# Kernel optimization log

Hardware: AMD Instinct MI355X
Metric: run time of the kernel (lower is better)

## Reference

```python
import jax, jax.numpy as jnp
import numpy as np
from jax import lax


def _pairwise_dist(a, b):
    # a: (T, D), b: (T, D) -> (T, T) Euclidean distances via GEMM trick
    a2 = jnp.sum(a * a, axis=-1)
    b2 = jnp.sum(b * b, axis=-1)
    sq = a2[:, None] + b2[None, :] - 2.0 * (a @ b.T)
    return jnp.sqrt(jnp.maximum(sq, 1e-12))


def _frechet(seq1, seq2):
    cost = _pairwise_dist(seq1, seq2)  # (T, T)
    ca0 = lax.cummax(cost[0])          # first row boundary: running max

    def row_step(prev, cost_row):
        # prev: ca[i-1, :]; cost_row: cost[i, :]
        c0 = jnp.maximum(prev[0], cost_row[0])  # first-column boundary

        def col_step(left, x):
            c, up, diag = x
            val = jnp.maximum(c, jnp.minimum(jnp.minimum(up, left), diag))
            return val, val

        _, rest = lax.scan(col_step, c0, (cost_row[1:], prev[1:], prev[:-1]))
        cur = jnp.concatenate([c0[None], rest])
        return cur, None

    final_row, _ = lax.scan(row_step, ca0, cost[1:])
    return final_row[-1]


def setup_inputs() -> dict:
    key = jax.random.key(0)
    k1, k2 = jax.random.split(key)
    B, T, D = 32, 1024, 64
    pred = jax.random.normal(k1, (B, T, D), dtype=jnp.float32)
    targ = jax.random.normal(k2, (B, T, D), dtype=jnp.float32)
    return {"pred": pred, "targ": targ}


def reference(pred, targ):
    dists = jax.vmap(_frechet)(pred, targ)  # (B,)
    return jnp.mean(dists)
```

## Files before the change

### kernel.cpp

```cpp
#include <hip/hip_runtime.h>
#include <hip/hip_fp16.h>
#include <hip/hip_bf16.h>
#include <math.h>

#define T_LEN 1024
#define D_DIM 64
#define BATCH 32

#define SLACK_FRONT 64
#define SLACK_BACK  72
#define ROW_STRIDE  (T_LEN + SLACK_FRONT)
#define PD 8

typedef __attribute__((ext_vector_type(2))) _Float16 h2v;

__global__ __launch_bounds__(256) void fill_slack_kernel(__half* __restrict__ ws) {
    int g = blockIdx.x * 256 + threadIdx.x;
    int b = g >> 13;
    int off = g & 8191;
    uint4* dst = (uint4*)(ws + (size_t)b * ((size_t)ROW_STRIDE * T_LEN)) + off;
    *dst = make_uint4(0x7C007C00u, 0x7C007C00u, 0x7C007C00u, 0x7C007C00u);
}

__global__ __launch_bounds__(256) void cost_kernel(const float* __restrict__ pred,
                                                   const float* __restrict__ targ,
                                                   __half* __restrict__ cost_base,
                                                   unsigned long long batch_stride_h) {
    const int b = blockIdx.z;
    const float* P = pred + (size_t)b * T_LEN * D_DIM;
    const float* T = targ + (size_t)b * T_LEN * D_DIM;
    __half* C = cost_base + (size_t)b * batch_stride_h;
    const int row0 = blockIdx.y * 128;
    const int col0 = blockIdx.x * 128;

    __shared__ __align__(16) float ps[32][132];
    __shared__ __align__(16) float ts[32][132];
    __shared__ float p2[128], t2[128];

    const int tid = threadIdx.x;

    {
        int r = tid & 127;
        const float* src = (tid < 128) ? (P + (size_t)(row0 + r) * D_DIM)
                                       : (T + (size_t)(col0 + r) * D_DIM);
        float s = 0.0f;
#pragma unroll
        for (int q = 0; q < 16; q++) {
            float4 v = ((const float4*)src)[q];
            s += v.x * v.x + v.y * v.y + v.z * v.z + v.w * v.w;
        }
        if (tid < 128) p2[r] = s; else t2[r] = s;
    }

    const int lane = tid & 63, wv = tid >> 6;
    const int TX = (lane & 7) + 8 * (wv & 1);
    const int TY = (lane >> 3) + 8 * (wv >> 1);

    float acc[8][8];
#pragma unroll
    for (int i = 0; i < 8; i++)
#pragma unroll
        for (int j = 0; j < 8; j++) acc[i][j] = 0.0f;

#pragma unroll
    for (int chunk = 0; chunk < 2; ++chunk) {
        __syncthreads();
#pragma unroll
        for (int it = 0; it < 4; ++it) {
            int idx = tid + 256 * it;
            int row = idx >> 3;
            int kc = idx & 7;
            float4 v = *(const float4*)(P + (size_t)(row0 + row) * D_DIM + 32 * chunk + 4 * kc);
            ps[4 * kc + 0][row] = v.x; ps[4 * kc + 1][row] = v.y;
            ps[4 * kc + 2][row] = v.z; ps[4 * kc + 3][row] = v.w;
            float4 w = *(const float4*)(T + (size_t)(col0 + row) * D_DIM + 32 * chunk + 4 * kc);
            ts[4 * kc + 0][row] = w.x; ts[4 * kc + 1][row] = w.y;
            ts[4 * kc + 2][row] = w.z; ts[4 * kc + 3][row] = w.w;
        }
        __syncthreads();

#pragma unroll
        for (int kk = 0; kk < 32; ++kk) {
            float4 a0 = *(const float4*)&ps[kk][8 * TY];
            float4 a1 = *(const float4*)&ps[kk][8 * TY + 4];
            float4 b0 = *(const float4*)&ts[kk][8 * TX];
            float4 b1 = *(const float4*)&ts[kk][8 * TX + 4];
            float av[8] = {a0.x, a0.y, a0.z, a0.w, a1.x, a1.y, a1.z, a1.w};
            float bv[8] = {b0.x, b0.y, b0.z, b0.w, b1.x, b1.y, b1.z, b1.w};
#pragma unroll
            for (int i = 0; i < 8; i++)
#pragma unroll
                for (int j = 0; j < 8; j++) acc[i][j] += av[i] * bv[j];
        }
    }
    __syncthreads();

#pragma unroll
    for (int i = 0; i < 8; i++) {
        float pa = p2[8 * TY + i];
        h2v o2[4];
#pragma unroll
        for (int j = 0; j < 4; j++) {
            float d0 = pa + t2[8 * TX + 2 * j]     - 2.0f * acc[i][2 * j];
            float d1 = pa + t2[8 * TX + 2 * j + 1] - 2.0f * acc[i][2 * j + 1];
            h2v h;
            h[0] = (_Float16)sqrtf(fmaxf(d0, 1e-12f));
            h[1] = (_Float16)sqrtf(fmaxf(d1, 1e-12f));
            o2[j] = h;
        }
        float4 st;
        st.x = __builtin_bit_cast(float, o2[0]);
        st.y = __builtin_bit_cast(float, o2[1]);
        st.z = __builtin_bit_cast(float, o2[2]);
        st.w = __builtin_bit_cast(float, o2[3]);
        __half* dst = C + (size_t)(row0 + 8 * TY + i) * T_LEN + col0 + 8 * TX;
        *(float4*)dst = st;
    }
}


#define CELL(c_, pv_) { \
    float c = (c_); \
    float e = fminf(pv_, diag); \
    float hm = fmaxf(e, c); \
    float vv = __builtin_amdgcn_fmed3f(c, hm, left); \
    diag = pv_; pv_ = vv; left = vv; }

#define DP_STEP(PA, PB) { \
    float inc = __shfl_up(right_out, 1, 64); \
    float left = (t == 0) ? lane0_left : inc; \
    float diag = (t == 0) ? INF : diag_feed; \
    diag_feed = inc; \
    h2v u0 = __builtin_bit_cast(h2v, PA.x), u1 = __builtin_bit_cast(h2v, PA.y); \
    h2v u2 = __builtin_bit_cast(h2v, PA.z), u3 = __builtin_bit_cast(h2v, PA.w); \
    h2v u4 = __builtin_bit_cast(h2v, PB.x), u5 = __builtin_bit_cast(h2v, PB.y); \
    h2v u6 = __builtin_bit_cast(h2v, PB.z), u7 = __builtin_bit_cast(h2v, PB.w); \
    CELL((float)u0[0], v0)  CELL((float)u0[1], v1) \
    CELL((float)u1[0], v2)  CELL((float)u1[1], v3) \
    CELL((float)u2[0], v4)  CELL((float)u2[1], v5) \
    CELL((float)u3[0], v6)  CELL((float)u3[1], v7) \
    CELL((float)u4[0], v8)  CELL((float)u4[1], v9) \
    CELL((float)u5[0], v10) CELL((float)u5[1], v11) \
    CELL((float)u6[0], v12) CELL((float)u6[1], v13) \
    CELL((float)u7[0], v14) CELL((float)u7[1], v15) \
    right_out = left; lane0_left = INF; }

#define RELOAD(n) { \
    const float4* p4 = (const float4*)q##n; \
    a##n = p4[0]; b##n = p4[1]; \
    q##n += (size_t)PD * T_LEN; }

#define INIT_SLOT(n) { \
    const float4* p4 = (const float4*)(Cl + (ptrdiff_t)(n - t) * T_LEN); \
    a##n = p4[0]; b##n = p4[1]; \
    q##n = Cl + (ptrdiff_t)(n + PD - t) * T_LEN; }

__global__ __launch_bounds__(64, 1) void dp_kernel_nb(const __half* __restrict__ cost,
                                                      float* __restrict__ out) {
    const int b = blockIdx.x;
    const int t = threadIdx.x;
    const float INF = __builtin_inff();
    const __half* Cl = cost + ((size_t)SLACK_FRONT + (size_t)b * ROW_STRIDE) * T_LEN + 16 * t;

    float v0 = INF, v1 = INF, v2 = INF, v3 = INF, v4 = INF, v5 = INF, v6 = INF, v7 = INF;
    float v8 = INF, v9 = INF, v10 = INF, v11 = INF, v12 = INF, v13 = INF, v14 = INF, v15 = INF;
    float right_out = INF;
    float diag_feed = INF;
    float lane0_left = -INF;

    float4 a0, b0, a1, b1, a2, b2, a3, b3, a4, b4, a5, b5, a6, b6, a7, b7;
    const __half *q0, *q1, *q2, *q3, *q4, *q5, *q6, *q7;
    INIT_SLOT(0) INIT_SLOT(1) INIT_SLOT(2) INIT_SLOT(3)
    INIT_SLOT(4) INIT_SLOT(5) INIT_SLOT(6) INIT_SLOT(7)

    for (int chunk = 0; chunk < 135; ++chunk) {
        DP_STEP(a0, b0) RELOAD(0)
        DP_STEP(a1, b1) RELOAD(1)
        DP_STEP(a2, b2) RELOAD(2)
        DP_STEP(a3, b3) RELOAD(3)
        DP_STEP(a4, b4) RELOAD(4)
        DP_STEP(a5, b5) RELOAD(5)
        DP_STEP(a6, b6) RELOAD(6)
        DP_STEP(a7, b7) RELOAD(7)
    }
    DP_STEP(a0, b0)
    DP_STEP(a1, b1)
    DP_STEP(a2, b2)
    DP_STEP(a3, b3)
    DP_STEP(a4, b4)
    DP_STEP(a5, b5)
    DP_STEP(a6, b6)

    if (t == 63) atomicAdd(out, v15 * (1.0f / (float)BATCH));
}

__global__ __launch_bounds__(64) void dp_fused_kernel(const float* __restrict__ pred,
                                                      const float* __restrict__ targ,
                                                      float* __restrict__ out) {
    const int b = blockIdx.x;
    const int t = threadIdx.x;
    const float INF = __builtin_inff();
    const float* P = pred + (size_t)b * T_LEN * D_DIM;
    const float* T = targ + (size_t)b * T_LEN * D_DIM + (size_t)(16 * t) * D_DIM;

    float prev[16];
#pragma unroll
    for (int j = 0; j < 16; j++) prev[j] = INF;
    float right_out = INF;
    float diag_feed = INF;

    for (int s = 0; s < T_LEN + 63; s++) {
        int r = s - t;
        float inc = __shfl_up(right_out, 1, 64);
        float left = inc, diag = diag_feed;
        diag_feed = inc;
        if (t == 0) { left = (r == 0) ? -INF : INF; diag = INF; }
        if (r >= 0 && r < T_LEN) {
            float4 pr[16];
            const float4* pp = (const float4*)(P + (size_t)r * D_DIM);
#pragma unroll
            for (int q = 0; q < 16; q++) pr[q] = pp[q];
#pragma unroll
            for (int j = 0; j < 16; j++) {
                const float4* tp = (const float4*)(T + (size_t)j * D_DIM);
                float acc = 0.0f;
#pragma unroll
                for (int q = 0; q < 16; q++) {
                    float4 tv = tp[q];
                    float dx = pr[q].x - tv.x; acc += dx * dx;
                    float dy = pr[q].y - tv.y; acc += dy * dy;
                    float dz = pr[q].z - tv.z; acc += dz * dz;
                    float dw = pr[q].w - tv.w; acc += dw * dw;
                }
                float c = sqrtf(fmaxf(acc, 1e-12f));
                float e = fminf(prev[j], diag);
                float hm = fmaxf(e, c);
                float vv = __builtin_amdgcn_fmed3f(c, hm, left);
                diag = prev[j];
                prev[j] = vv;
                left = vv;
            }
            right_out = left;
        }
    }
    if (t == 63) atomicAdd(out, prev[15] * (1.0f / (float)BATCH));
}

extern "C" void kernel_launch(void* const* d_in, const int* in_sizes, int n_in,
                              void* d_out, int out_size, void* d_ws, size_t ws_size,
                              hipStream_t stream) {
    const float* pred = (const float*)d_in[0];
    const float* targ = (const float*)d_in[1];
    float* out = (float*)d_out;

    hipMemsetAsync(out, 0, sizeof(float) * out_size, stream);

    const size_t need_strided =
        ((size_t)BATCH * ROW_STRIDE + SLACK_BACK) * (size_t)T_LEN * sizeof(__half);

    if (ws_size >= need_strided) {
        __half* ws = (__half*)d_ws;
        fill_slack_kernel<<<1024, 256, 0, stream>>>(ws);
        __half* cost_base = ws + (size_t)SLACK_FRONT * T_LEN;
        dim3 grid(8, 8, BATCH);
        cost_kernel<<<grid, 256, 0, stream>>>(pred, targ, cost_base,
                                              (unsigned long long)ROW_STRIDE * T_LEN);
        dp_kernel_nb<<<BATCH, 64, 0, stream>>>(ws, out);
    } else {
        dp_fused_kernel<<<BATCH, 64, 0, stream>>>(pred, targ, out);
    }
}
```

Measured before the change: 368.5 us.

## Skew cost matrix storage, run DP recurrence in fp16, pin reload scheduling

The cost kernel now writes each 16-column strip shifted down by its lane index, so every DP wavefront step reads one contiguous skewed row. Only the upper-left staircase is filled with +inf, which replaces the full slack-fill pass. The DP recurrence now keeps its state in _Float16 with half min/max/med3 operations and shuffles 16-bit values, and sched_barriers fence each reload. Doing the min/max in fp16 could change rounding and ties compared with the fp32 path, and the fused fallback swaps fmed3 for a max/min pair.

```diff
diff --git a/kernel.cpp b/kernel.cpp
--- a/kernel.cpp
+++ b/kernel.cpp
@@ -1,35 +1,58 @@
 #include <hip/hip_runtime.h>
 #include <hip/hip_fp16.h>
-#include <hip/hip_bf16.h>
 #include <math.h>
 
 #define T_LEN 1024
 #define D_DIM 64
 #define BATCH 32
 
-#define SLACK_FRONT 64
-#define SLACK_BACK  72
-#define ROW_STRIDE  (T_LEN + SLACK_FRONT)
+#define SKEW_ROWS 1104
+#define SKEW_STRIDE ((size_t)SKEW_ROWS * T_LEN)
 #define PD 8
 
 typedef __attribute__((ext_vector_type(2))) _Float16 h2v;
 
-__global__ __launch_bounds__(256) void fill_slack_kernel(__half* __restrict__ ws) {
-    int g = blockIdx.x * 256 + threadIdx.x;
-    int b = g >> 13;
-    int off = g & 8191;
-    uint4* dst = (uint4*)(ws + (size_t)b * ((size_t)ROW_STRIDE * T_LEN)) + off;
-    *dst = make_uint4(0x7C007C00u, 0x7C007C00u, 0x7C007C00u, 0x7C007C00u);
+static __device__ __forceinline__ _Float16 hmin_(_Float16 a, _Float16 b) {
+#if __has_builtin(__builtin_fminf16)
+    return __builtin_fminf16(a, b);
+#else
+    return (b < a) ? b : a;
+#endif
+}
+static __device__ __forceinline__ _Float16 hmax_(_Float16 a, _Float16 b) {
+#if __has_builtin(__builtin_fmaxf16)
+    return __builtin_fmaxf16(a, b);
+#else
+    return (a < b) ? b : a;
+#endif
+}
+static __device__ __forceinline__ _Float16 med3h_(_Float16 a, _Float16 b, _Float16 c) {
+#if __has_builtin(__builtin_amdgcn_fmed3h)
+    return __builtin_amdgcn_fmed3h(a, b, c);
+#else
+    return hmax_(a, hmin_(b, c));
+#endif
+}
+
+__global__ __launch_bounds__(128) void fill_stairs_kernel(__half* __restrict__ ws) {
+    int s = blockIdx.x;
+    int b = blockIdx.y;
+    int tid = threadIdx.x;
+    int col0 = 16 * (s + 1);
+    int n_u4 = (T_LEN - col0) >> 3;
+    if (tid < n_u4) {
+        __half* row = ws + (size_t)b * SKEW_STRIDE + (size_t)s * T_LEN + col0;
+        ((uint4*)row)[tid] = make_uint4(0x7C007C00u, 0x7C007C00u, 0x7C007C00u, 0x7C007C00u);
+    }
 }
 
 __global__ __launch_bounds__(256) void cost_kernel(const float* __restrict__ pred,
                                                    const float* __restrict__ targ,
-                                                   __half* __restrict__ cost_base,
-                                                   unsigned long long batch_stride_h) {
+                                                   __half* __restrict__ skew_base) {
     const int b = blockIdx.z;
     const float* P = pred + (size_t)b * T_LEN * D_DIM;
     const float* T = targ + (size_t)b * T_LEN * D_DIM;
-    __half* C = cost_base + (size_t)b * batch_stride_h;
+    __half* C = skew_base + (size_t)b * SKEW_STRIDE;
     const int row0 = blockIdx.y * 128;
     const int col0 = blockIdx.x * 128;
 
@@ -95,6 +118,7 @@
     }
     __syncthreads();
 
+    const int skew = (col0 >> 4) + (TX >> 1);
 #pragma unroll
     for (int i = 0; i < 8; i++) {
         float pa = p2[8 * TY + i];
@@ -113,66 +137,67 @@
         st.y = __builtin_bit_cast(float, o2[1]);
         st.z = __builtin_bit_cast(float, o2[2]);
         st.w = __builtin_bit_cast(float, o2[3]);
-        __half* dst = C + (size_t)(row0 + 8 * TY + i) * T_LEN + col0 + 8 * TX;
+        __half* dst = C + (size_t)(row0 + 8 * TY + i + skew) * T_LEN + col0 + 8 * TX;
         *(float4*)dst = st;
     }
 }
 
 
 #define CELL(c_, pv_) { \
-    float c = (c_); \
-    float e = fminf(pv_, diag); \
-    float hm = fmaxf(e, c); \
-    float vv = __builtin_amdgcn_fmed3f(c, hm, left); \
+    _Float16 c = (c_); \
+    _Float16 e = hmin_(pv_, diag); \
+    _Float16 hm = hmax_(e, c); \
+    _Float16 vv = med3h_(c, hm, left); \
     diag = pv_; pv_ = vv; left = vv; }
 
 #define DP_STEP(PA, PB) { \
-    float inc = __shfl_up(right_out, 1, 64); \
-    float left = (t == 0) ? lane0_left : inc; \
-    float diag = (t == 0) ? INF : diag_feed; \
-    diag_feed = inc; \
+    int inc = __shfl_up(ro_bits, 1, 64); \
+    _Float16 inch = __builtin_bit_cast(_Float16, (unsigned short)inc); \
+    _Float16 left = (t == 0) ? lane0_left : inch; \
+    _Float16 diag = (t == 0) ? HINF : diag_feed; \
+    diag_feed = inch; \
     h2v u0 = __builtin_bit_cast(h2v, PA.x), u1 = __builtin_bit_cast(h2v, PA.y); \
     h2v u2 = __builtin_bit_cast(h2v, PA.z), u3 = __builtin_bit_cast(h2v, PA.w); \
     h2v u4 = __builtin_bit_cast(h2v, PB.x), u5 = __builtin_bit_cast(h2v, PB.y); \
     h2v u6 = __builtin_bit_cast(h2v, PB.z), u7 = __builtin_bit_cast(h2v, PB.w); \
-    CELL((float)u0[0], v0)  CELL((float)u0[1], v1) \
-    CELL((float)u1[0], v2)  CELL((float)u1[1], v3) \
-    CELL((float)u2[0], v4)  CELL((float)u2[1], v5) \
-    CELL((float)u3[0], v6)  CELL((float)u3[1], v7) \
-    CELL((float)u4[0], v8)  CELL((float)u4[1], v9) \
-    CELL((float)u5[0], v10) CELL((float)u5[1], v11) \
-    CELL((float)u6[0], v12) CELL((float)u6[1], v13) \
-    CELL((float)u7[0], v14) CELL((float)u7[1], v15) \
-    right_out = left; lane0_left = INF; }
+    CELL(u0[0], v0)  CELL(u0[1], v1)  CELL(u1[0], v2)  CELL(u1[1], v3) \
+    CELL(u2[0], v4)  CELL(u2[1], v5)  CELL(u3[0], v6)  CELL(u3[1], v7) \
+    CELL(u4[0], v8)  CELL(u4[1], v9)  CELL(u5[0], v10) CELL(u5[1], v11) \
+    CELL(u6[0], v12) CELL(u6[1], v13) CELL(u7[0], v14) CELL(u7[1], v15) \
+    ro_bits = (int)(unsigned)__builtin_bit_cast(unsigned short, left); \
+    lane0_left = HINF; }
 
 #define RELOAD(n) { \
-    const float4* p4 = (const float4*)q##n; \
+    __builtin_amdgcn_sched_barrier(0); \
+    { const float4* p4 = (const float4*)q##n; \
+      a##n = p4[0]; b##n = p4[1]; \
+      q##n += (size_t)PD * T_LEN; } \
+    __builtin_amdgcn_sched_barrier(0); }
+
+#define INIT_SLOT(n) { \
+    const float4* p4 = (const float4*)(Lp + (size_t)n * T_LEN); \
     a##n = p4[0]; b##n = p4[1]; \
-    q##n += (size_t)PD * T_LEN; }
-
-#define INIT_SLOT(n) { \
-    const float4* p4 = (const float4*)(Cl + (ptrdiff_t)(n - t) * T_LEN); \
-    a##n = p4[0]; b##n = p4[1]; \
-    q##n = Cl + (ptrdiff_t)(n + PD - t) * T_LEN; }
+    q##n = Lp + (size_t)(n + PD) * T_LEN; }
 
 __global__ __launch_bounds__(64, 1) void dp_kernel_nb(const __half* __restrict__ cost,
                                                       float* __restrict__ out) {
     const int b = blockIdx.x;
     const int t = threadIdx.x;
-    const float INF = __builtin_inff();
-    const __half* Cl = cost + ((size_t)SLACK_FRONT + (size_t)b * ROW_STRIDE) * T_LEN + 16 * t;
-
-    float v0 = INF, v1 = INF, v2 = INF, v3 = INF, v4 = INF, v5 = INF, v6 = INF, v7 = INF;
-    float v8 = INF, v9 = INF, v10 = INF, v11 = INF, v12 = INF, v13 = INF, v14 = INF, v15 = INF;
-    float right_out = INF;
-    float diag_feed = INF;
-    float lane0_left = -INF;
+    const _Float16 HINF = __builtin_bit_cast(_Float16, (unsigned short)0x7C00);
+    const __half* Lp = cost + (size_t)b * SKEW_STRIDE + 16 * t;
+
+    _Float16 v0 = HINF, v1 = HINF, v2 = HINF, v3 = HINF, v4 = HINF, v5 = HINF, v6 = HINF, v7 = HINF;
+    _Float16 v8 = HINF, v9 = HINF, v10 = HINF, v11 = HINF, v12 = HINF, v13 = HINF, v14 = HINF, v15 = HINF;
+    _Float16 diag_feed = HINF;
+    _Float16 lane0_left = __builtin_bit_cast(_Float16, (unsigned short)0xFC00);
+    int ro_bits = 0x7C00;
 
     float4 a0, b0, a1, b1, a2, b2, a3, b3, a4, b4, a5, b5, a6, b6, a7, b7;
     const __half *q0, *q1, *q2, *q3, *q4, *q5, *q6, *q7;
     INIT_SLOT(0) INIT_SLOT(1) INIT_SLOT(2) INIT_SLOT(3)
     INIT_SLOT(4) INIT_SLOT(5) INIT_SLOT(6) INIT_SLOT(7)
 
+#pragma unroll 1
     for (int chunk = 0; chunk < 135; ++chunk) {
         DP_STEP(a0, b0) RELOAD(0)
         DP_STEP(a1, b1) RELOAD(1)
@@ -191,7 +216,7 @@
     DP_STEP(a5, b5)
     DP_STEP(a6, b6)
 
-    if (t == 63) atomicAdd(out, v15 * (1.0f / (float)BATCH));
+    if (t == 63) atomicAdd(out, (float)v15 * (1.0f / (float)BATCH));
 }
 
 __global__ __launch_bounds__(64) void dp_fused_kernel(const float* __restrict__ pred,
@@ -235,7 +260,7 @@
                 float c = sqrtf(fmaxf(acc, 1e-12f));
                 float e = fminf(prev[j], diag);
                 float hm = fmaxf(e, c);
-                float vv = __builtin_amdgcn_fmed3f(c, hm, left);
+                float vv = fmaxf(c, fminf(hm, left));
                 diag = prev[j];
                 prev[j] = vv;
                 left = vv;
@@ -255,16 +280,12 @@
 
     hipMemsetAsync(out, 0, sizeof(float) * out_size, stream);
 
-    const size_t need_strided =
-        ((size_t)BATCH * ROW_STRIDE + SLACK_BACK) * (size_t)T_LEN * sizeof(__half);
-
-    if (ws_size >= need_strided) {
+    const size_t need = (size_t)BATCH * SKEW_STRIDE * sizeof(__half);
+
+    if (ws_size >= need) {
         __half* ws = (__half*)d_ws;
-        fill_slack_kernel<<<1024, 256, 0, stream>>>(ws);
-        __half* cost_base = ws + (size_t)SLACK_FRONT * T_LEN;
-        dim3 grid(8, 8, BATCH);
-        cost_kernel<<<grid, 256, 0, stream>>>(pred, targ, cost_base,
-                                              (unsigned long long)ROW_STRIDE * T_LEN);
+        fill_stairs_kernel<<<dim3(63, 32), 128, 0, stream>>>(ws);
+        cost_kernel<<<dim3(8, 8, BATCH), 256, 0, stream>>>(pred, targ, ws);
         dp_kernel_nb<<<BATCH, 64, 0, stream>>>(ws, out);
     } else {
         dp_fused_kernel<<<BATCH, 64, 0, stream>>>(pred, targ, out);
```

Result: slower. 381.5 us (+3.5%).
